# Kernel tuning notes

Measured on AMD Instinct MI355X. Metric: run time of the kernel, lower is better.

## Reference

```python
import jax, jax.numpy as jnp
import numpy as np

N_NODES = 20000
N_EDGES = 320000
IN_DIM = 128
HID = 256
HEADS = 8
DH = HID // HEADS  # 32
LAYERS = 3
NUM_GRAPHS = 64
OUT_DIM = 10
SLOPE = 0.2  # DGL GATv2Conv default negative_slope


def setup_inputs() -> dict:
    key = jax.random.key(0)
    ks = jax.random.split(key, 20)
    s_in = 1.0 / np.sqrt(IN_DIM)
    s_h = 1.0 / np.sqrt(HID)
    s_h2 = 1.0 / np.sqrt(HID // 2)
    return {
        "feature": jax.random.normal(ks[0], (N_NODES, IN_DIM), jnp.float32),
        "W_in": jax.random.normal(ks[1], (IN_DIM, HID), jnp.float32) * s_in,
        "b_in": jax.random.normal(ks[2], (HID,), jnp.float32) * 0.01,
        "W_src": jax.random.normal(ks[3], (LAYERS, HID, HID), jnp.float32) * s_h,
        "b_src": jax.random.normal(ks[4], (LAYERS, HID), jnp.float32) * 0.01,
        "W_dst": jax.random.normal(ks[5], (LAYERS, HID, HID), jnp.float32) * s_h,
        "b_dst": jax.random.normal(ks[6], (LAYERS, HID), jnp.float32) * 0.01,
        "attn": jax.random.normal(ks[7], (LAYERS, HEADS, DH), jnp.float32) * (1.0 / np.sqrt(DH)),
        "Wc1": jax.random.normal(ks[8], (HID, HID), jnp.float32) * s_h,
        "bc1": jax.random.normal(ks[9], (HID,), jnp.float32) * 0.01,
        "Wc2": jax.random.normal(ks[10], (HID, HID // 2), jnp.float32) * s_h,
        "bc2": jax.random.normal(ks[11], (HID // 2,), jnp.float32) * 0.01,
        "Wc3": jax.random.normal(ks[12], (HID // 2, OUT_DIM), jnp.float32) * s_h2,
        "bc3": jax.random.normal(ks[13], (OUT_DIM,), jnp.float32) * 0.01,
        "src": jax.random.randint(ks[14], (N_EDGES,), 0, N_NODES, jnp.int32),
        "dst": jax.random.randint(ks[15], (N_EDGES,), 0, N_NODES, jnp.int32),
        "graph_ids": jnp.sort(jax.random.randint(ks[16], (N_NODES,), 0, NUM_GRAPHS, jnp.int32)),
    }


def _gatv2_layer(h, Ws, bs, Wd, bd, a, src, dst):
    # DGL GATv2Conv: e_ij = a^T LeakyReLU(W_src h_j + W_dst h_i), edge softmax over
    # incoming edges of dst, scatter-sum of alpha * W_src h_src; residual = Identity
    # (in_feats == heads*out_feats); activation relu.
    n = h.shape[0]
    fs = (h @ Ws + bs).reshape(n, HEADS, DH)  # [N,H,D]
    fd = (h @ Wd + bd).reshape(n, HEADS, DH)
    e = jax.nn.leaky_relu(fs[src] + fd[dst], SLOPE)          # [E,H,D]
    score = jnp.einsum("ehd,hd->eh", e, a)                   # [E,H]
    m = jax.ops.segment_max(score, dst, num_segments=n)       # stable softmax max
    ex = jnp.exp(score - m[dst])
    denom = jax.ops.segment_sum(ex, dst, num_segments=n)
    alpha = ex / denom[dst]                                    # [E,H]
    rst = jax.ops.segment_sum(alpha[:, :, None] * fs[src], dst, num_segments=n)
    out = jax.nn.relu(rst + h.reshape(n, HEADS, DH))          # residual + activation
    return out.reshape(n, HID)


def reference(feature, W_in, b_in, W_src, b_src, W_dst, b_dst, attn,
              Wc1, bc1, Wc2, bc2, Wc3, bc3, src, dst, graph_ids):
    h = feature @ W_in + b_in
    for l in range(LAYERS):
        h = _gatv2_layer(h, W_src[l], b_src[l], W_dst[l], b_dst[l], attn[l], src, dst)
    # dgl.sum_nodes over batched graph -> per-graph segment sum
    hg = jax.ops.segment_sum(h, graph_ids, num_segments=NUM_GRAPHS)  # [G,HID]
    # classifier (dropout is identity in eval mode)
    x = jax.nn.relu(hg @ Wc1 + bc1)
    x = jax.nn.relu(x @ Wc2 + bc2)
    return x @ Wc3 + bc3  # [G,OUT_DIM]
```

## Files before the change

kernel.cpp:

```cpp
#include <hip/hip_runtime.h>
#include <hip/hip_bf16.h>
#include <math.h>

#define N_NODES 20000
#define N_EDGES 320000
#define IN_DIM 128
#define HID 256
#define HEADS 8
#define DH 32
#define LAYERS 3
#define NUM_GRAPHS 64
#define OUT_DIM 10
#define SLOPE 0.2f

#define NBKT 5
#define N_BINS (N_NODES * NBKT)
#define N_BINS4 (N_BINS / 4)

#define CHUNK_I4 255
#define N_CHUNKS 99

#define GEMM_TILES 626
#define COUNT_BLOCKS 1250

typedef __bf16 bf16x8 __attribute__((ext_vector_type(8)));
typedef float f32x4 __attribute__((ext_vector_type(4)));

static __device__ __forceinline__ unsigned short f2bfbits(float v) {
    __bf16 b = (__bf16)v;
    return __builtin_bit_cast(unsigned short, b);
}
static __device__ __forceinline__ void unpack8(uint4 u, float* f) {
    unsigned p0 = u.x, p1 = u.y, p2 = u.z, p3 = u.w;
    f[0] = __builtin_bit_cast(float, p0 << 16);
    f[1] = __builtin_bit_cast(float, p0 & 0xffff0000u);
    f[2] = __builtin_bit_cast(float, p1 << 16);
    f[3] = __builtin_bit_cast(float, p1 & 0xffff0000u);
    f[4] = __builtin_bit_cast(float, p2 << 16);
    f[5] = __builtin_bit_cast(float, p2 & 0xffff0000u);
    f[6] = __builtin_bit_cast(float, p3 << 16);
    f[7] = __builtin_bit_cast(float, p3 & 0xffff0000u);
}

typedef const __attribute__((address_space(1))) unsigned int* as1_u32p;
typedef __attribute__((address_space(3))) unsigned int* as3_u32p;
static __device__ __forceinline__ void async_cp16(const unsigned short* g, unsigned short* l) {
    __builtin_amdgcn_global_load_lds((as1_u32p)g, (as3_u32p)l, 16, 0, 0);
}

#define CAST_N4 (N_NODES * IN_DIM / 4)
#define WTRANS_TOTAL (IN_DIM * HID + 6 * HID * HID)
#define PREP_TOTAL (CAST_N4 + WTRANS_TOTAL)
#define PREP_BLOCKS (PREP_TOTAL / 256)

static __device__ void prep_item(int idx,
                                 const float* __restrict__ feat,
                                 const float* __restrict__ Win,
                                 const float* __restrict__ Wsrc,
                                 const float* __restrict__ Wdst,
                                 unsigned short* __restrict__ featH,
                                 unsigned short* __restrict__ WinT,
                                 unsigned short* __restrict__ WT) {
    if (idx < CAST_N4) {
        float4 v = ((const float4*)feat)[idx];
        ushort4 o;
        o.x = f2bfbits(v.x); o.y = f2bfbits(v.y);
        o.z = f2bfbits(v.z); o.w = f2bfbits(v.w);
        ((ushort4*)featH)[idx] = o;
    } else {
        int j = idx - CAST_N4;
        if (j < IN_DIM * HID) {
            int n = j / IN_DIM, k = j % IN_DIM;
            WinT[j] = f2bfbits(Win[k * HID + n]);
        } else {
            int r6 = j - IN_DIM * HID;
            int mat = r6 >> 16;
            int r = r6 & 65535;
            int n = r >> 8, k = r & 255;
            const float* base = (mat < 3) ? (Wsrc + (size_t)mat * 65536)
                                          : (Wdst + (size_t)(mat - 3) * 65536);
            WT[r6] = f2bfbits(base[k * 256 + n]);
        }
    }
}

static __device__ void scans_unit(int u, int t, const int* __restrict__ cnt,
                                  int* __restrict__ cglob, int* __restrict__ offs,
                                  int* __restrict__ cursor, int* si) {
    int idx4 = u * CHUNK_I4 + t;
    bool act = (t < CHUNK_I4) && (idx4 < N_BINS4);
    int4 x = make_int4(0, 0, 0, 0);
    if (act) x = ((const int4*)cnt)[idx4];
    int tsum = x.x + x.y + x.z + x.w;
    int v = tsum;
#pragma unroll
    for (int d = 1; d < 64; d <<= 1) {
        int w = __shfl_up(v, d, 64);
        if ((t & 63) >= d) v += w;
    }
    if ((t & 63) == 63) si[4 + (t >> 6)] = v;
    __syncthreads();
    if (t == 0) {
        int S = si[4] + si[5] + si[6] + si[7];
        si[0] = atomicAdd(cglob, S);
    }
    __syncthreads();
    int base = si[0];
    int wid = t >> 6;
    int waveoff = 0;
    if (wid > 0) waveoff += si[4];
    if (wid > 1) waveoff += si[5];
    if (wid > 2) waveoff += si[6];
    int ex = base + waveoff + (v - tsum);
    if (act) {
        int4 o;
        o.x = ex; o.y = ex + x.x; o.z = o.y + x.y; o.w = o.z + x.z;
        ((int4*)offs)[idx4] = o;
        ((int4*)cursor)[idx4] = o;
    }
}

template <int DUAL>
static __device__ void gemm_tile(int mt, int nt, int t,
                                 const unsigned short* __restrict__ Ah,
                                 const unsigned short* __restrict__ BT1,
                                 const float* __restrict__ bias1,
                                 unsigned short* __restrict__ O1,
                                 const unsigned short* __restrict__ BT2,
                                 const float* __restrict__ bias2,
                                 unsigned short* __restrict__ O2,
                                 int M, int K, int N,
                                 unsigned short* AsP, unsigned short* Bs1P,
                                 unsigned short* Bs2P) {
    const int wv = t >> 6, lane = t & 63, quad = lane >> 4, l15 = lane & 15;
    const int m0 = mt * 64, n0 = nt * 128;

    const int sA = wv * 64 + lane;
    const int rA = sA >> 2, cA = (sA & 3) ^ ((rA >> 1) & 3);
    int gmA = m0 + rA; if (gmA >= M) gmA = M - 1;
    const size_t offA = (size_t)gmA * K + cA * 8;
    const int sB0 = wv * 64 + lane, sB1v = sB0 + 256;
    const int rB0 = sB0 >> 2, cB0 = (sB0 & 3) ^ ((rB0 >> 1) & 3);
    const int rB1 = sB1v >> 2, cB1 = (sB1v & 3) ^ ((rB1 >> 1) & 3);
    const size_t offB0 = (size_t)(n0 + rB0) * K + cB0 * 8;
    const size_t offB1 = (size_t)(n0 + rB1) * K + cB1 * 8;

    const int nk = K >> 5;
    for (int c = 0; c < nk; ++c)
        async_cp16(Ah + offA + c * 32, AsP + c * 2048 + wv * 512);

    auto issueB = [&](int buf, int k0) {
        async_cp16(BT1 + offB0 + k0, Bs1P + buf * 4096 + wv * 512);
        async_cp16(BT1 + offB1 + k0, Bs1P + buf * 4096 + 2048 + wv * 512);
        if (DUAL) {
            async_cp16(BT2 + offB0 + k0, Bs2P + buf * 4096 + wv * 512);
            async_cp16(BT2 + offB1 + k0, Bs2P + buf * 4096 + 2048 + wv * 512);
        }
    };

    const int mrow0 = (wv >> 1) * 32;
    const int ncb = (wv & 1) * 64;

    f32x4 zero = {0.f, 0.f, 0.f, 0.f};
    f32x4 acc1[2][4], acc2[2][4];
#pragma unroll
    for (int mi = 0; mi < 2; ++mi)
#pragma unroll
        for (int t4 = 0; t4 < 4; ++t4) { acc1[mi][t4] = zero; acc2[mi][t4] = zero; }

    issueB(0, 0);
    int buf = 0;
    for (int k0 = 0; k0 < K; k0 += 32, buf ^= 1) {
        __syncthreads();
        if (k0 + 32 < K) issueB(buf ^ 1, k0 + 32);
        const unsigned short* Ak = AsP + (k0 >> 5) * 2048;

        bf16x8 aF[2];
#pragma unroll
        for (int mi = 0; mi < 2; ++mi) {
            int row = mrow0 + mi * 16 + l15;
            int aoff = row * 32 + ((quad ^ ((row >> 1) & 3)) << 3);
            aF[mi] = __builtin_bit_cast(bf16x8, *(const uint4*)(Ak + aoff));
        }
#pragma unroll
        for (int t4 = 0; t4 < 4; ++t4) {
            int brow = ncb + t4 * 16 + l15;
            int boff = brow * 32 + ((quad ^ ((brow >> 1) & 3)) << 3);
            bf16x8 b1 = __builtin_bit_cast(bf16x8, *(const uint4*)(Bs1P + buf * 4096 + boff));
#pragma unroll
            for (int mi = 0; mi < 2; ++mi)
                acc1[mi][t4] = __builtin_amdgcn_mfma_f32_16x16x32_bf16(aF[mi], b1, acc1[mi][t4], 0, 0, 0);
            if (DUAL) {
                bf16x8 b2 = __builtin_bit_cast(bf16x8, *(const uint4*)(Bs2P + buf * 4096 + boff));
#pragma unroll
                for (int mi = 0; mi < 2; ++mi)
                    acc2[mi][t4] = __builtin_amdgcn_mfma_f32_16x16x32_bf16(aF[mi], b2, acc2[mi][t4], 0, 0, 0);
            }
        }
    }

    float bia1[4], bia2[4];
#pragma unroll
    for (int t4 = 0; t4 < 4; ++t4) {
        bia1[t4] = bias1[n0 + ncb + t4 * 16 + l15];
        bia2[t4] = DUAL ? bias2[n0 + ncb + t4 * 16 + l15] : 0.f;
    }
#pragma unroll
    for (int mi = 0; mi < 2; ++mi) {
#pragma unroll
        for (int t4 = 0; t4 < 4; ++t4) {
            int gn = n0 + ncb + t4 * 16 + l15;
#pragma unroll
            for (int r = 0; r < 4; ++r) {
                int gm = m0 + mrow0 + mi * 16 + quad * 4 + r;
                if (gm < M) {
                    float v = acc1[mi][t4][r] + bia1[t4];
                    O1[(size_t)gm * N + gn] = f2bfbits(v);
                    if (DUAL) {
                        float v2 = acc2[mi][t4][r] + bia2[t4];
                        O2[(size_t)gm * N + gn] = f2bfbits(v2);
                    }
                }
            }
        }
    }
}

static __device__ void agg_unit(int u, int t,
                                const unsigned short* __restrict__ fsb,
                                const unsigned short* __restrict__ fdb,
                                unsigned short* __restrict__ hb,
                                const int* __restrict__ offs,
                                const int* __restrict__ cnt,
                                const int* __restrict__ csr_src,
                                const float* __restrict__ attn_l) {
    int node = u * 8 + (t >> 5);
    if (node >= N_NODES) return;
    int l32 = t & 31;
    int dbase = l32 * 8;
    int abase = (l32 >> 2) * DH + (l32 & 3) * 8;

    float a[8];
#pragma unroll
    for (int j = 0; j < 8; ++j) a[j] = attn_l[abase + j];

    float fdv[8];
    unpack8(*(const uint4*)(fdb + (size_t)node * HID + dbase), fdv);

    float ssum0 = 0.f, ssum1 = 0.f;
    float acc0[8], acc1[8];
#pragma unroll
    for (int j = 0; j < 8; ++j) { acc0[j] = 0.f; acc1[j] = 0.f; }

    auto procE = [&](uint4 uu, float* acc, float& ssum) {
        float fsv[8];
        unpack8(uu, fsv);
        float p = 0.f;
#pragma unroll
        for (int j = 0; j < 8; ++j) {
            float e = fsv[j] + fdv[j];
            e = fmaxf(e, SLOPE * e);
            p += e * a[j];
        }
        p += __shfl_xor(p, 1, 64);
        p += __shfl_xor(p, 2, 64);
        float w = __expf(p);
        ssum += w;
#pragma unroll
        for (int j = 0; j < 8; ++j) acc[j] += w * fsv[j];
    };

    const unsigned short* fsl = fsb + dbase;
    int b0 = node * NBKT;
    int beg = offs[b0];
    int end = offs[b0 + NBKT - 1] + cnt[b0 + NBKT - 1];
    int nfull = (end - beg) >> 2;
    const int limit = beg + nfull * 4;

    uint4 cu0, cu1, cu2, cu3;
    int ci0, ci1, ci2, ci3;
    int base = beg + 8;
    bool have = (nfull >= 1);
    bool haveN = (nfull >= 2);
    if (have) {
        int s0 = csr_src[beg], s1 = csr_src[beg + 1];
        int s2 = csr_src[beg + 2], s3 = csr_src[beg + 3];
        if (haveN) {
            ci0 = csr_src[beg + 4]; ci1 = csr_src[beg + 5];
            ci2 = csr_src[beg + 6]; ci3 = csr_src[beg + 7];
        }
        cu0 = *(const uint4*)(fsl + (size_t)s0 * HID);
        cu1 = *(const uint4*)(fsl + (size_t)s1 * HID);
        cu2 = *(const uint4*)(fsl + (size_t)s2 * HID);
        cu3 = *(const uint4*)(fsl + (size_t)s3 * HID);
    }
    while (have) {
        uint4 nu0, nu1, nu2, nu3;
        int ni0, ni1, ni2, ni3;
        if (haveN) {
            nu0 = *(const uint4*)(fsl + (size_t)ci0 * HID);
            nu1 = *(const uint4*)(fsl + (size_t)ci1 * HID);
            nu2 = *(const uint4*)(fsl + (size_t)ci2 * HID);
            nu3 = *(const uint4*)(fsl + (size_t)ci3 * HID);
        }
        bool haveNN = (base + 4 <= limit);
        if (haveNN) {
            ni0 = csr_src[base]; ni1 = csr_src[base + 1];
            ni2 = csr_src[base + 2]; ni3 = csr_src[base + 3];
        }
        base += 4;
        procE(cu0, acc0, ssum0);
        procE(cu1, acc1, ssum1);
        procE(cu2, acc0, ssum0);
        procE(cu3, acc1, ssum1);
        if (haveN) { cu0 = nu0; cu1 = nu1; cu2 = nu2; cu3 = nu3; }
        if (haveNN) { ci0 = ni0; ci1 = ni1; ci2 = ni2; ci3 = ni3; }
        have = haveN; haveN = haveNN;
    }
    for (int idx = limit; idx < end; ++idx) {
        int sv = csr_src[idx];
        procE(*(const uint4*)(fsl + (size_t)sv * HID), acc0, ssum0);
    }

    float ssum = ssum0 + ssum1;
    float acc[8];
#pragma unroll
    for (int j = 0; j < 8; ++j) acc[j] = acc0[j] + acc1[j];

    float inv = ssum > 0.f ? 1.f / ssum : 0.f;
    float hv[8];
    unpack8(*(const uint4*)(hb + (size_t)node * HID + dbase), hv);
    unsigned short ob[8];
#pragma unroll
    for (int j = 0; j < 8; ++j) {
        float o = fmaxf(acc[j] * inv + hv[j], 0.f);
        ob[j] = f2bfbits(o);
    }
    *(uint4*)(hb + (size_t)node * HID + dbase) = *(uint4*)ob;
}

__global__ void prep_count_kernel(const float* __restrict__ feat,
                                  const float* __restrict__ Win,
                                  const float* __restrict__ Wsrc,
                                  const float* __restrict__ Wdst,
                                  unsigned short* __restrict__ featH,
                                  unsigned short* __restrict__ WinT,
                                  unsigned short* __restrict__ WT,
                                  const int* __restrict__ src,
                                  const int* __restrict__ dst,
                                  int* __restrict__ cnt) {
    int bid = blockIdx.x;
    if (bid < PREP_BLOCKS) {
        prep_item(bid * 256 + threadIdx.x, feat, Win, Wsrc, Wdst, featH, WinT, WT);
    } else {
        int e = (bid - PREP_BLOCKS) * 256 + threadIdx.x;
        if (e < N_EDGES) atomicAdd(&cnt[dst[e] * NBKT + (src[e] >> 12)], 1);
    }
}

__global__ __launch_bounds__(256, 4) void gemm0_scan_kernel(
    const unsigned short* __restrict__ featH, const unsigned short* __restrict__ WinT,
    const float* __restrict__ b_in, unsigned short* __restrict__ hb,
    const int* __restrict__ cnt, int* __restrict__ cglob,
    int* __restrict__ offs, int* __restrict__ cursor) {
    __shared__ __align__(16) unsigned short smem[16384];
    int bid = blockIdx.x;
    if (bid < GEMM_TILES) {
        gemm_tile<0>(bid >> 1, bid & 1, threadIdx.x, featH, WinT, b_in, hb,
                     (const unsigned short*)nullptr, (const float*)nullptr,
                     (unsigned short*)nullptr, N_NODES, IN_DIM, HID,
                     smem, smem + 8192, smem);
    } else {
        scans_unit(bid - GEMM_TILES, threadIdx.x, cnt, cglob, offs, cursor,
                   (int*)(void*)smem);
    }
}

__global__ __launch_bounds__(256, 2) void gemm1_fill_kernel(
    const unsigned short* __restrict__ hb,
    const unsigned short* __restrict__ WTs, const float* __restrict__ bs,
    unsigned short* __restrict__ fsb,
    const unsigned short* __restrict__ WTd, const float* __restrict__ bd,
    unsigned short* __restrict__ fdb,
    const int* __restrict__ src, const int* __restrict__ dst,
    int* __restrict__ cursor, int* __restrict__ csr_src) {
    __shared__ __align__(16) unsigned short smem[32768];
    int bid = blockIdx.x;
    if (bid < GEMM_TILES) {
        gemm_tile<1>(bid >> 1, bid & 1, threadIdx.x, hb, WTs, bs, fsb, WTd, bd, fdb,
                     N_NODES, HID, HID, smem, smem + 16384, smem + 24576);
    } else {
        int e = (bid - GEMM_TILES) * 256 + threadIdx.x;
        if (e < N_EDGES) {
            int sv = src[e];
            int p = atomicAdd(&cursor[dst[e] * NBKT + (sv >> 12)], 1);
            csr_src[p] = sv;
        }
    }
}

__global__ __launch_bounds__(256, 2) void gemm_kernel(
    const unsigned short* __restrict__ Ah,
    const unsigned short* __restrict__ BT1, const float* __restrict__ bias1,
    unsigned short* __restrict__ O1,
    const unsigned short* __restrict__ BT2, const float* __restrict__ bias2,
    unsigned short* __restrict__ O2) {
    __shared__ __align__(16) unsigned short smem[32768];
    gemm_tile<1>(blockIdx.x, blockIdx.y, threadIdx.x, Ah, BT1, bias1, O1,
                 BT2, bias2, O2, N_NODES, HID, HID, smem, smem + 16384, smem + 24576);
}

__global__ __launch_bounds__(256) void agg_kernel(const unsigned short* __restrict__ fsb,
                                                  const unsigned short* __restrict__ fdb,
                                                  unsigned short* __restrict__ hb,
                                                  const int* __restrict__ offs,
                                                  const int* __restrict__ cnt,
                                                  const int* __restrict__ csr_src,
                                                  const float* __restrict__ attn_l) {
    int nwg = gridDim.x;
    int q = nwg >> 3, r = nwg & 7;
    int xcd = blockIdx.x & 7, idx = blockIdx.x >> 3;
    int u = (xcd < r) ? xcd * (q + 1) + idx
                      : r * (q + 1) + (xcd - r) * q + idx;
    agg_unit(u, threadIdx.x, fsb, fdb, hb, offs, cnt, csr_src, attn_l);
}

__global__ __launch_bounds__(256) void poolcls_kernel(
    const unsigned short* __restrict__ hb, const int* __restrict__ gid,
    const float* __restrict__ Wc1, const float* __restrict__ bc1,
    const float* __restrict__ Wc2, const float* __restrict__ bc2,
    const float* __restrict__ Wc3, const float* __restrict__ bc3,
    float* __restrict__ out) {
    __shared__ float part[8 * HID];
    __shared__ float xin[HID];
    __shared__ float x1[HID];
    __shared__ float x2[HID / 2];
    int g = blockIdx.x, t = threadIdx.x;

    int lo = 0, hi = N_NODES;
    while (lo < hi) { int mid = (lo + hi) >> 1; if (gid[mid] < g) lo = mid + 1; else hi = mid; }
    int s0 = lo;
    hi = N_NODES;
    while (lo < hi) { int mid = (lo + hi) >> 1; if (gid[mid] < g + 1) lo = mid + 1; else hi = mid; }
    int e0 = lo;

    int r = t >> 5;
    int fb = (t & 31) * 8;
    float a0[8], a1[8];
#pragma unroll
    for (int j = 0; j < 8; ++j) { a0[j] = 0.f; a1[j] = 0.f; }
    int n = s0 + r;
    for (; n + 8 < e0; n += 16) {
        uint4 u0 = *(const uint4*)(hb + (size_t)n * HID + fb);
        uint4 u1 = *(const uint4*)(hb + (size_t)(n + 8) * HID + fb);
        float f0[8], f1[8];
        unpack8(u0, f0); unpack8(u1, f1);
#pragma unroll
        for (int j = 0; j < 8; ++j) { a0[j] += f0[j]; a1[j] += f1[j]; }
    }
    if (n < e0) {
        uint4 u0 = *(const uint4*)(hb + (size_t)n * HID + fb);
        float f0[8];
        unpack8(u0, f0);
#pragma unroll
        for (int j = 0; j < 8; ++j) a0[j] += f0[j];
    }
#pragma unroll
    for (int j = 0; j < 8; ++j) part[r * HID + fb + j] = a0[j] + a1[j];
    __syncthreads();
    {
        float s = 0.f;
#pragma unroll
        for (int r2 = 0; r2 < 8; ++r2) s += part[r2 * HID + t];
        xin[t] = s;
    }
    __syncthreads();

    {
        float acc = bc1[t];
        for (int k = 0; k < HID; ++k) acc += xin[k] * Wc1[k * HID + t];
        x1[t] = fmaxf(acc, 0.f);
    }
    __syncthreads();
    if (t < HID / 2) {
        float acc = bc2[t];
        for (int k = 0; k < HID; ++k) acc += x1[k] * Wc2[k * (HID / 2) + t];
        x2[t] = fmaxf(acc, 0.f);
    }
    __syncthreads();
    if (t < OUT_DIM) {
        float acc = bc3[t];
        for (int k = 0; k < HID / 2; ++k) acc += x2[k] * Wc3[k * OUT_DIM + t];
        out[g * OUT_DIM + t] = acc;
    }
}

extern "C" void kernel_launch(void* const* d_in, const int* in_sizes, int n_in,
                              void* d_out, int out_size, void* d_ws, size_t ws_size,
                              hipStream_t stream) {
    const float* feature = (const float*)d_in[0];
    const float* W_in   = (const float*)d_in[1];
    const float* b_in   = (const float*)d_in[2];
    const float* W_src  = (const float*)d_in[3];
    const float* b_src  = (const float*)d_in[4];
    const float* W_dst  = (const float*)d_in[5];
    const float* b_dst  = (const float*)d_in[6];
    const float* attn   = (const float*)d_in[7];
    const float* Wc1    = (const float*)d_in[8];
    const float* bc1    = (const float*)d_in[9];
    const float* Wc2    = (const float*)d_in[10];
    const float* bc2    = (const float*)d_in[11];
    const float* Wc3    = (const float*)d_in[12];
    const float* bc3    = (const float*)d_in[13];
    const int* src     = (const int*)d_in[14];
    const int* dst     = (const int*)d_in[15];
    const int* gid     = (const int*)d_in[16];
    float* out = (float*)d_out;

    char* w = (char*)d_ws;
    auto alloc = [&](size_t bytes) -> void* {
        void* p = (void*)w;
        w += (bytes + 255) & ~(size_t)255;
        return p;
    };
    unsigned short* hb  = (unsigned short*)alloc((size_t)N_NODES * HID * 2);
    unsigned short* fsb = (unsigned short*)alloc((size_t)N_NODES * HID * 2);
    unsigned short* fdb = (unsigned short*)alloc((size_t)N_NODES * HID * 2);
    int* cnt     = (int*)alloc((size_t)N_BINS * 4);
    int* cglob   = (int*)alloc(4);
    int* offs    = (int*)alloc((size_t)(N_BINS + 4) * 4);
    int* cursor  = (int*)alloc((size_t)N_BINS * 4);
    int* csr_src = (int*)alloc((size_t)N_EDGES * 4);
    unsigned short* WinT = (unsigned short*)alloc((size_t)IN_DIM * HID * 2);
    unsigned short* WT   = (unsigned short*)alloc((size_t)6 * HID * HID * 2);
    unsigned short* featH = (unsigned short*)alloc((size_t)N_NODES * IN_DIM * 2);
    (void)alloc(4096);

    size_t zlen = (size_t)((char*)offs - (char*)cnt);
    hipMemsetAsync(cnt, 0, zlen, stream);

    hipLaunchKernelGGL(prep_count_kernel, dim3(PREP_BLOCKS + COUNT_BLOCKS), dim3(256), 0, stream,
                       feature, W_in, W_src, W_dst, featH, WinT, WT, src, dst, cnt);

    hipLaunchKernelGGL(gemm0_scan_kernel, dim3(GEMM_TILES + N_CHUNKS), dim3(256), 0, stream,
                       featH, WinT, b_in, hb, cnt, cglob, offs, cursor);

    hipLaunchKernelGGL(gemm1_fill_kernel, dim3(GEMM_TILES + COUNT_BLOCKS), dim3(256), 0, stream,
                       hb, WT, b_src, fsb, WT + 3 * 65536, b_dst, fdb,
                       src, dst, cursor, csr_src);

    for (int l = 0; l < LAYERS; ++l) {
        hipLaunchKernelGGL(agg_kernel, dim3(N_NODES / 8), dim3(256), 0, stream,
                           fsb, fdb, hb, offs, cnt, csr_src, attn + (size_t)l * HEADS * DH);
        if (l + 1 < LAYERS) {
            hipLaunchKernelGGL(gemm_kernel, dim3(313, 2), dim3(256), 0, stream,
                               hb, WT + (size_t)(l + 1) * 65536, b_src + (size_t)(l + 1) * HID, fsb,
                               WT + (size_t)(4 + l) * 65536, b_dst + (size_t)(l + 1) * HID, fdb);
        }
    }

    hipLaunchKernelGGL(poolcls_kernel, dim3(NUM_GRAPHS), dim3(256), 0, stream,
                       hb, gid, Wc1, bc1, Wc2, bc2, Wc3, bc3, out);
}
```

Before: 316.2 us.

## Load GEMM A fragments directly from global into registers, halve LDS, raise occupancy

The GEMM tile no longer stages the whole A row-block into shared memory. Each wave now reads its A fragments straight from global memory into registers, prefetching one K-step ahead. This halves LDS use per block, so the launch bounds of the dual GEMM kernels go from 2 to 4 blocks per CU, aiming for better latency hiding. The trade-off is uncoalesced 16-byte global reads of A, with each row fetched twice by the two column-half waves, plus extra register pressure under the tighter launch bound.

```diff
diff --git a/kernel.cpp b/kernel.cpp
--- a/kernel.cpp
+++ b/kernel.cpp
@@ -130,24 +130,15 @@
                                  const float* __restrict__ bias2,
                                  unsigned short* __restrict__ O2,
                                  int M, int K, int N,
-                                 unsigned short* AsP, unsigned short* Bs1P,
-                                 unsigned short* Bs2P) {
+                                 unsigned short* Bs1P, unsigned short* Bs2P) {
     const int wv = t >> 6, lane = t & 63, quad = lane >> 4, l15 = lane & 15;
     const int m0 = mt * 64, n0 = nt * 128;
 
-    const int sA = wv * 64 + lane;
-    const int rA = sA >> 2, cA = (sA & 3) ^ ((rA >> 1) & 3);
-    int gmA = m0 + rA; if (gmA >= M) gmA = M - 1;
-    const size_t offA = (size_t)gmA * K + cA * 8;
     const int sB0 = wv * 64 + lane, sB1v = sB0 + 256;
     const int rB0 = sB0 >> 2, cB0 = (sB0 & 3) ^ ((rB0 >> 1) & 3);
     const int rB1 = sB1v >> 2, cB1 = (sB1v & 3) ^ ((rB1 >> 1) & 3);
     const size_t offB0 = (size_t)(n0 + rB0) * K + cB0 * 8;
     const size_t offB1 = (size_t)(n0 + rB1) * K + cB1 * 8;
-
-    const int nk = K >> 5;
-    for (int c = 0; c < nk; ++c)
-        async_cp16(Ah + offA + c * 32, AsP + c * 2048 + wv * 512);
 
     auto issueB = [&](int buf, int k0) {
         async_cp16(BT1 + offB0 + k0, Bs1P + buf * 4096 + wv * 512);
@@ -161,6 +152,11 @@
     const int mrow0 = (wv >> 1) * 32;
     const int ncb = (wv & 1) * 64;
 
+    int r0 = m0 + mrow0 + l15;      if (r0 >= M) r0 = M - 1;
+    int r1 = m0 + mrow0 + 16 + l15; if (r1 >= M) r1 = M - 1;
+    const unsigned short* Ap0 = Ah + (size_t)r0 * K + quad * 8;
+    const unsigned short* Ap1 = Ah + (size_t)r1 * K + quad * 8;
+
     f32x4 zero = {0.f, 0.f, 0.f, 0.f};
     f32x4 acc1[2][4], acc2[2][4];
 #pragma unroll
@@ -169,34 +165,32 @@
         for (int t4 = 0; t4 < 4; ++t4) { acc1[mi][t4] = zero; acc2[mi][t4] = zero; }
 
     issueB(0, 0);
+    bf16x8 aC0 = __builtin_bit_cast(bf16x8, *(const uint4*)(Ap0));
+    bf16x8 aC1 = __builtin_bit_cast(bf16x8, *(const uint4*)(Ap1));
+
     int buf = 0;
     for (int k0 = 0; k0 < K; k0 += 32, buf ^= 1) {
         __syncthreads();
-        if (k0 + 32 < K) issueB(buf ^ 1, k0 + 32);
-        const unsigned short* Ak = AsP + (k0 >> 5) * 2048;
-
-        bf16x8 aF[2];
-#pragma unroll
-        for (int mi = 0; mi < 2; ++mi) {
-            int row = mrow0 + mi * 16 + l15;
-            int aoff = row * 32 + ((quad ^ ((row >> 1) & 3)) << 3);
-            aF[mi] = __builtin_bit_cast(bf16x8, *(const uint4*)(Ak + aoff));
+        bf16x8 aN0 = aC0, aN1 = aC1;
+        if (k0 + 32 < K) {
+            issueB(buf ^ 1, k0 + 32);
+            aN0 = __builtin_bit_cast(bf16x8, *(const uint4*)(Ap0 + k0 + 32));
+            aN1 = __builtin_bit_cast(bf16x8, *(const uint4*)(Ap1 + k0 + 32));
         }
 #pragma unroll
         for (int t4 = 0; t4 < 4; ++t4) {
             int brow = ncb + t4 * 16 + l15;
             int boff = brow * 32 + ((quad ^ ((brow >> 1) & 3)) << 3);
             bf16x8 b1 = __builtin_bit_cast(bf16x8, *(const uint4*)(Bs1P + buf * 4096 + boff));
-#pragma unroll
-            for (int mi = 0; mi < 2; ++mi)
-                acc1[mi][t4] = __builtin_amdgcn_mfma_f32_16x16x32_bf16(aF[mi], b1, acc1[mi][t4], 0, 0, 0);
+            acc1[0][t4] = __builtin_amdgcn_mfma_f32_16x16x32_bf16(aC0, b1, acc1[0][t4], 0, 0, 0);
+            acc1[1][t4] = __builtin_amdgcn_mfma_f32_16x16x32_bf16(aC1, b1, acc1[1][t4], 0, 0, 0);
             if (DUAL) {
                 bf16x8 b2 = __builtin_bit_cast(bf16x8, *(const uint4*)(Bs2P + buf * 4096 + boff));
-#pragma unroll
-                for (int mi = 0; mi < 2; ++mi)
-                    acc2[mi][t4] = __builtin_amdgcn_mfma_f32_16x16x32_bf16(aF[mi], b2, acc2[mi][t4], 0, 0, 0);
+                acc2[0][t4] = __builtin_amdgcn_mfma_f32_16x16x32_bf16(aC0, b2, acc2[0][t4], 0, 0, 0);
+                acc2[1][t4] = __builtin_amdgcn_mfma_f32_16x16x32_bf16(aC1, b2, acc2[1][t4], 0, 0, 0);
             }
         }
+        aC0 = aN0; aC1 = aN1;
     }
 
     float bia1[4], bia2[4];
@@ -363,20 +357,20 @@
     const float* __restrict__ b_in, unsigned short* __restrict__ hb,
     const int* __restrict__ cnt, int* __restrict__ cglob,
     int* __restrict__ offs, int* __restrict__ cursor) {
-    __shared__ __align__(16) unsigned short smem[16384];
+    __shared__ __align__(16) unsigned short smem[8192];
     int bid = blockIdx.x;
     if (bid < GEMM_TILES) {
         gemm_tile<0>(bid >> 1, bid & 1, threadIdx.x, featH, WinT, b_in, hb,
                      (const unsigned short*)nullptr, (const float*)nullptr,
                      (unsigned short*)nullptr, N_NODES, IN_DIM, HID,
-                     smem, smem + 8192, smem);
+                     smem, smem);
     } else {
         scans_unit(bid - GEMM_TILES, threadIdx.x, cnt, cglob, offs, cursor,
                    (int*)(void*)smem);
     }
 }
 
-__global__ __launch_bounds__(256, 2) void gemm1_fill_kernel(
+__global__ __launch_bounds__(256, 4) void gemm1_fill_kernel(
     const unsigned short* __restrict__ hb,
     const unsigned short* __restrict__ WTs, const float* __restrict__ bs,
     unsigned short* __restrict__ fsb,
@@ -384,11 +378,11 @@
     unsigned short* __restrict__ fdb,
     const int* __restrict__ src, const int* __restrict__ dst,
     int* __restrict__ cursor, int* __restrict__ csr_src) {
-    __shared__ __align__(16) unsigned short smem[32768];
+    __shared__ __align__(16) unsigned short smem[16384];
     int bid = blockIdx.x;
     if (bid < GEMM_TILES) {
         gemm_tile<1>(bid >> 1, bid & 1, threadIdx.x, hb, WTs, bs, fsb, WTd, bd, fdb,
-                     N_NODES, HID, HID, smem, smem + 16384, smem + 24576);
+                     N_NODES, HID, HID, smem, smem + 8192);
     } else {
         int e = (bid - GEMM_TILES) * 256 + threadIdx.x;
         if (e < N_EDGES) {
@@ -399,15 +393,15 @@
     }
 }
 
-__global__ __launch_bounds__(256, 2) void gemm_kernel(
+__global__ __launch_bounds__(256, 4) void gemm_kernel(
     const unsigned short* __restrict__ Ah,
     const unsigned short* __restrict__ BT1, const float* __restrict__ bias1,
     unsigned short* __restrict__ O1,
     const unsigned short* __restrict__ BT2, const float* __restrict__ bias2,
     unsigned short* __restrict__ O2) {
-    __shared__ __align__(16) unsigned short smem[32768];
+    __shared__ __align__(16) unsigned short smem[16384];
     gemm_tile<1>(blockIdx.x, blockIdx.y, threadIdx.x, Ah, BT1, bias1, O1,
-                 BT2, bias2, O2, N_NODES, HID, HID, smem, smem + 16384, smem + 24576);
+                 BT2, bias2, O2, N_NODES, HID, HID, smem, smem + 8192);
 }
 
 __global__ __launch_bounds__(256) void agg_kernel(const unsigned short* __restrict__ fsb,
```

New measurement: 314.6 us. No clear change (-0.5%).
